# Kernel optimization log

Hardware: AMD Instinct MI355X
Metric: run time of the kernel (lower is better)

Reference implementation:

```python
import jax, jax.numpy as jnp
import numpy as np

VOCAB = 90000
MAX_ID = 95000
EFFECT_DIM = 758
ADD_DIM = 10
EMBED_DIM = 768  # EFFECT_DIM + ADD_DIM
CTX = 1024
MAX_SYN = 8


def setup_inputs() -> dict:
    key = jax.random.key(0)
    k_ids, k_emb, k_rev, k_tab, k_msk = jax.random.split(key, 5)
    ids = jax.random.randint(k_ids, (CTX,), 0, VOCAB, dtype=jnp.int64)
    W_emb = jax.random.normal(k_emb, (MAX_ID, EFFECT_DIM), dtype=jnp.float32)
    W_rev = jax.random.normal(k_rev, (EMBED_DIM, MAX_ID), dtype=jnp.float32)
    padding = 0.1 * jnp.ones((CTX, ADD_DIM), dtype=jnp.float32)
    # synonym ids live in [VOCAB, MAX_ID); only some slots are active (variable-length lists)
    syn_table = jax.random.randint(k_tab, (MAX_ID, MAX_SYN), VOCAB, MAX_ID, dtype=jnp.int32)
    syn_mask = jax.random.randint(k_msk, (MAX_ID, MAX_SYN), 0, 2, dtype=jnp.int32)
    # tokens >= VOCAB (synonym ids themselves) have no synonyms
    syn_mask = syn_mask.at[VOCAB:].set(0)
    return {"ids": ids, "W_emb": W_emb, "W_rev": W_rev, "padding": padding,
            "syn_table": syn_table, "syn_mask": syn_mask}


def reference(ids, W_emb, W_rev, padding, syn_table, syn_mask):
    # VirtualEmbedding: base gather + masked synonym gather/scale/accumulate.
    # i_sum is computed BEFORE the synonym loop in the original, so each
    # synonym contribution is independent -> vectorized masked reduction.
    # (Dropout in eval mode is the identity.)
    base = W_emb[ids]                              # [L, D]
    syn_ids = syn_table[ids]                       # [L, K]
    syn = W_emb[syn_ids]                           # [L, K, D]
    mask = syn_mask[ids].astype(base.dtype)        # [L, K]
    i_sum = jnp.sum(base, axis=-1, keepdims=True)  # [L, 1]
    s_sum = jnp.sum(syn, axis=-1)                  # [L, K]
    d = i_sum / s_sum                              # [L, K]
    emb = base + jnp.einsum('lk,lkd->ld', mask * d, syn)
    # concat fixed context padding, then ReverseEmbedding projection to vocab
    full = jnp.concatenate([emb, padding], axis=1)  # [L, EMBED_DIM]
    return full @ W_rev                             # [L, MAX_ID]
```

## Files before the change

kernel.cpp:

```cpp
#include <hip/hip_runtime.h>
#include <stdint.h>

#define EFFECT_DIM 758
#define ADD_DIM 10
#define EMBED_DIM 768
#define NCOLS 95000
#define NSYN 8
#define NROWS 1024
#define NTILE_N 743

typedef __attribute__((ext_vector_type(8))) __bf16 bf16x8;
typedef __attribute__((ext_vector_type(16))) float f32x16;
typedef __attribute__((ext_vector_type(4))) uint32_t u32x4;

static __device__ __forceinline__ uint32_t pack2(float a, float b) {
  uint32_t r;
  asm("v_cvt_pk_bf16_f32 %0, %1, %2" : "=v"(r) : "v"(a), "v"(b));
  return r;
}

__global__ __launch_bounds__(256) void emb_kernel(
    const int* __restrict__ ids, const float* __restrict__ W_emb,
    const float* __restrict__ padding, const int* __restrict__ syn_table,
    const int* __restrict__ syn_mask, char* __restrict__ ws)
{
  const int l = blockIdx.x;
  const int t = threadIdx.x;
  const int id = ids[l];
  int sid[NSYN];
  int msk[NSYN];
#pragma unroll
  for (int k = 0; k < NSYN; ++k) {
    sid[k] = syn_table[id * NSYN + k];
    msk[k] = syn_mask[id * NSYN + k];
  }

  double p[9] = {0, 0, 0, 0, 0, 0, 0, 0, 0};
  for (int d = t; d < EFFECT_DIM; d += 256) {
    p[0] += (double)W_emb[(size_t)id * EFFECT_DIM + d];
#pragma unroll
    for (int k = 0; k < NSYN; ++k)
      p[k + 1] += (double)W_emb[(size_t)sid[k] * EFFECT_DIM + d];
  }

  __shared__ double s_red[9][4];
  const int w = t >> 6;
#pragma unroll
  for (int k = 0; k < 9; ++k) {
    double v = p[k];
#pragma unroll
    for (int off = 32; off > 0; off >>= 1) v += __shfl_down(v, off, 64);
    if ((t & 63) == 0) s_red[k][w] = v;
  }
  __syncthreads();

  const double isum = s_red[0][0] + s_red[0][1] + s_red[0][2] + s_red[0][3];
  float coef[NSYN];
#pragma unroll
  for (int k = 0; k < NSYN; ++k) {
    double ss = s_red[k + 1][0] + s_red[k + 1][1] + s_red[k + 1][2] + s_red[k + 1][3];
    coef[k] = msk[k] ? (float)(isum / ss) : 0.0f;
  }

  const int mt = l >> 7;
  const int r  = l & 127;
  const int sw = (r & 7) << 4;
  char* wbase = ws + (size_t)mt * (12 * 16384);

  for (int j = t; j < 384; j += 256) {
    const int d0 = 2 * j;
    float v0, v1;
    if (d0 < EFFECT_DIM) {
      const float* bp = W_emb + (size_t)id * EFFECT_DIM + d0;
      v0 = bp[0];
      v1 = bp[1];
#pragma unroll
      for (int k = 0; k < NSYN; ++k) {
        const float* sp = W_emb + (size_t)sid[k] * EFFECT_DIM + d0;
        v0 = fmaf(coef[k], sp[0], v0);
        v1 = fmaf(coef[k], sp[1], v1);
      }
    } else {
      v0 = padding[l * ADD_DIM + (d0 - EFFECT_DIM)];
      v1 = padding[l * ADD_DIM + (d0 + 1 - EFFECT_DIM)];
    }
    const int ks = j >> 5;
    const int jl = j & 31;
    *(uint32_t*)(wbase + ks * 16384 + r * 128 + ((jl * 4) ^ sw)) = pack2(v0, v1);
  }
}

__global__ __launch_bounds__(256) void conv_kernel(
    const float* __restrict__ Wrev, char* __restrict__ Bbuf)
{
  __shared__ char lds[16384];
  const int t  = threadIdx.x;
  const int nt = blockIdx.x;
  const int ks = blockIdx.y;

  const int nl = t & 127;
  const int kc_base = t >> 7;
  const int gn = nt * 128 + nl;
  const bool valid = gn < NCOLS;
  const int sw = (nl & 7) << 4;

#pragma unroll
  for (int task = 0; task < 4; ++task) {
    const int kc = kc_base + task * 2;
    float v[8];
    const float* p = Wrev + (size_t)(ks * 64 + kc * 8) * NCOLS + gn;
#pragma unroll
    for (int j = 0; j < 8; ++j)
      v[j] = valid ? p[(size_t)j * NCOLS] : 0.0f;
    u32x4 u;
#pragma unroll
    for (int j = 0; j < 4; ++j)
      u[j] = pack2(v[2 * j], v[2 * j + 1]);
    *(u32x4*)(lds + nl * 128 + ((kc * 16) ^ sw)) = u;
  }
  __syncthreads();

  char* dst = Bbuf + (size_t)(nt * 12 + ks) * 16384;
#pragma unroll
  for (int i = 0; i < 4; ++i)
    *(u32x4*)(dst + t * 16 + i * 4096) = *(const u32x4*)(lds + t * 16 + i * 4096);
}

__global__ __launch_bounds__(256, 4) void gemm_pre(
    const char* __restrict__ Abuf, const char* __restrict__ Bbuf,
    float* __restrict__ out)
{
  __shared__ char lds[32768];
  const int t  = threadIdx.x;
  const int l  = t & 63;
  const int w  = t >> 6;
  const int wm = w >> 1;
  const int wn = w & 1;
  const int lr = l & 31;
  const int lh = l >> 5;
  const int mt = blockIdx.x;
  const int nt = blockIdx.y;
  const int n0 = nt * 128;

  f32x16 acc[2][2] = {};

  const char* asrc = Abuf + (size_t)mt * (12 * 16384);
  const char* bsrc = Bbuf + (size_t)nt * (12 * 16384);

  for (int ks = 0; ks < 12; ++ks) {
    {
      const char* sa = asrc + ks * 16384 + w * 1024 + l * 16;
      const char* sb = bsrc + ks * 16384 + w * 1024 + l * 16;
      char* da = lds + w * 1024;
      char* db = lds + 16384 + w * 1024;
#pragma unroll
      for (int i = 0; i < 4; ++i) {
        __builtin_amdgcn_global_load_lds(
            (const __attribute__((address_space(1))) uint32_t*)(sa + i * 4096),
            (__attribute__((address_space(3))) uint32_t*)(da + i * 4096),
            16, 0, 0);
        __builtin_amdgcn_global_load_lds(
            (const __attribute__((address_space(1))) uint32_t*)(sb + i * 4096),
            (__attribute__((address_space(3))) uint32_t*)(db + i * 4096),
            16, 0, 0);
      }
    }
    __syncthreads();

    bf16x8 af[2][4], bg[2][4];
#pragma unroll
    for (int mr = 0; mr < 2; ++mr) {
      const int rr = wm * 64 + mr * 32 + lr;
      const int swz = (rr & 7) << 4;
#pragma unroll
      for (int kk = 0; kk < 4; ++kk) {
        const int c2 = kk * 32 + lh * 16;
        af[mr][kk] = *(const bf16x8*)(lds + rr * 128 + (c2 ^ swz));
      }
    }
#pragma unroll
    for (int nr = 0; nr < 2; ++nr) {
      const int rr = wn * 64 + nr * 32 + lr;
      const int swz = (rr & 7) << 4;
#pragma unroll
      for (int kk = 0; kk < 4; ++kk) {
        const int c2 = kk * 32 + lh * 16;
        bg[nr][kk] = *(const bf16x8*)(lds + 16384 + rr * 128 + (c2 ^ swz));
      }
    }
#pragma unroll
    for (int kk = 0; kk < 4; ++kk)
#pragma unroll
      for (int mr = 0; mr < 2; ++mr)
#pragma unroll
        for (int nr = 0; nr < 2; ++nr)
          acc[mr][nr] = __builtin_amdgcn_mfma_f32_32x32x16_bf16(
              af[mr][kk], bg[nr][kk], acc[mr][nr], 0, 0, 0);
    __syncthreads();
  }

#pragma unroll
  for (int mr = 0; mr < 2; ++mr)
#pragma unroll
    for (int nr = 0; nr < 2; ++nr) {
      const int gc = n0 + wn * 64 + nr * 32 + lr;
      if (gc < NCOLS) {
#pragma unroll
        for (int reg = 0; reg < 16; ++reg) {
          const int row = (reg & 3) + 8 * (reg >> 2) + 4 * lh;
          const int gr = mt * 128 + wm * 64 + mr * 32 + row;
          out[(size_t)gr * NCOLS + gc] = acc[mr][nr][reg];
        }
      }
    }
}

__global__ __launch_bounds__(256, 2) void gemm_kernel(
    const float* __restrict__ Wrev, const char* __restrict__ Abuf,
    float* __restrict__ out)
{
  __shared__ char lds[32768];
  const int t  = threadIdx.x;
  const int l  = t & 63;
  const int w  = t >> 6;
  const int wm = w >> 1;
  const int wn = w & 1;
  const int lr = l & 31;
  const int lh = l >> 5;
  const int mt = blockIdx.x;
  const int n0 = blockIdx.y * 128;

  f32x16 acc[2][2] = {};

  const char* asrc = Abuf + (size_t)mt * (12 * 16384);
  const int nl = t & 127;
  const int kc_base = t >> 7;
  const int gn = n0 + nl;
  const int bswz = (nl & 7) << 4;

  for (int ks = 0; ks < 12; ++ks) {
    {
      const char* s = asrc + ks * 16384 + w * 1024 + l * 16;
      char* d = lds + w * 1024;
#pragma unroll
      for (int i = 0; i < 4; ++i) {
        __builtin_amdgcn_global_load_lds(
            (const __attribute__((address_space(1))) uint32_t*)(s + i * 4096),
            (__attribute__((address_space(3))) uint32_t*)(d + i * 4096),
            16, 0, 0);
      }
    }
#pragma unroll
    for (int task = 0; task < 4; ++task) {
      const int kc = kc_base + task * 2;
      float v[8];
      const float* p = Wrev + (size_t)(ks * 64 + kc * 8) * NCOLS + gn;
#pragma unroll
      for (int j = 0; j < 8; ++j)
        v[j] = (gn < NCOLS) ? p[(size_t)j * NCOLS] : 0.0f;
      u32x4 u;
#pragma unroll
      for (int j = 0; j < 4; ++j)
        u[j] = pack2(v[2 * j], v[2 * j + 1]);
      *(u32x4*)(lds + 16384 + nl * 128 + ((kc * 16) ^ bswz)) = u;
    }
    __syncthreads();

    bf16x8 af[2][4], bg[2][4];
#pragma unroll
    for (int mr = 0; mr < 2; ++mr) {
      const int rr = wm * 64 + mr * 32 + lr;
      const int swz = (rr & 7) << 4;
#pragma unroll
      for (int kk = 0; kk < 4; ++kk) {
        const int c2 = kk * 32 + lh * 16;
        af[mr][kk] = *(const bf16x8*)(lds + rr * 128 + (c2 ^ swz));
      }
    }
#pragma unroll
    for (int nr = 0; nr < 2; ++nr) {
      const int rr = wn * 64 + nr * 32 + lr;
      const int swz = (rr & 7) << 4;
#pragma unroll
      for (int kk = 0; kk < 4; ++kk) {
        const int c2 = kk * 32 + lh * 16;
        bg[nr][kk] = *(const bf16x8*)(lds + 16384 + rr * 128 + (c2 ^ swz));
      }
    }
#pragma unroll
    for (int kk = 0; kk < 4; ++kk)
#pragma unroll
      for (int mr = 0; mr < 2; ++mr)
#pragma unroll
        for (int nr = 0; nr < 2; ++nr)
          acc[mr][nr] = __builtin_amdgcn_mfma_f32_32x32x16_bf16(
              af[mr][kk], bg[nr][kk], acc[mr][nr], 0, 0, 0);
    __syncthreads();
  }

#pragma unroll
  for (int mr = 0; mr < 2; ++mr)
#pragma unroll
    for (int nr = 0; nr < 2; ++nr) {
      const int gc = n0 + wn * 64 + nr * 32 + lr;
      if (gc < NCOLS) {
#pragma unroll
        for (int reg = 0; reg < 16; ++reg) {
          const int row = (reg & 3) + 8 * (reg >> 2) + 4 * lh;
          const int gr = mt * 128 + wm * 64 + mr * 32 + row;
          out[(size_t)gr * NCOLS + gc] = acc[mr][nr][reg];
        }
      }
    }
}

extern "C" void kernel_launch(void* const* d_in, const int* in_sizes, int n_in,
                              void* d_out, int out_size, void* d_ws, size_t ws_size,
                              hipStream_t stream) {
  const int*   ids       = (const int*)d_in[0];
  const float* W_emb     = (const float*)d_in[1];
  const float* W_rev     = (const float*)d_in[2];
  const float* padding   = (const float*)d_in[3];
  const int*   syn_table = (const int*)d_in[4];
  const int*   syn_mask  = (const int*)d_in[5];
  float* out = (float*)d_out;
  char*  ws  = (char*)d_ws;

  const size_t A_BYTES = (size_t)8 * 12 * 16384;
  const size_t B_BYTES = (size_t)NTILE_N * 12 * 16384;

  hipLaunchKernelGGL(emb_kernel, dim3(NROWS), dim3(256), 0, stream,
                     ids, W_emb, padding, syn_table, syn_mask, ws);

  if (ws_size >= A_BYTES + B_BYTES) {
    char* Bbuf = ws + A_BYTES;
    hipLaunchKernelGGL(conv_kernel, dim3(NTILE_N, 12), dim3(256), 0, stream,
                       W_rev, Bbuf);
    hipLaunchKernelGGL(gemm_pre, dim3(8, NTILE_N), dim3(256), 0, stream,
                       ws, Bbuf, out);
  } else {
    hipLaunchKernelGGL(gemm_kernel, dim3(8, NTILE_N), dim3(256), 0, stream,
                       W_rev, ws, out);
  }
}
```

Measured before the change: 357.2 us.

## Double-buffer LDS in pre-converted GEMM and remap workgroups per XCD

The pre-converted GEMM now keeps two LDS stages, so the async global-to-LDS load for the next K-step is issued before the current step's MFMAs, with explicit vmcnt waits and raw barriers in place of syncthreads. It also boosts wave priority around the MFMA block and uses a 1D grid whose IDs are remapped so that workgroups on one XCD share neighbouring N tiles and the same A tiles, for better L2 reuse. The larger LDS footprint lowers the occupancy bound from 4 to 2 blocks per CU, which could offset the overlap gain.

```diff
diff --git a/kernel.cpp b/kernel.cpp
--- a/kernel.cpp
+++ b/kernel.cpp
@@ -18,6 +18,11 @@
   asm("v_cvt_pk_bf16_f32 %0, %1, %2" : "=v"(r) : "v"(a), "v"(b));
   return r;
 }
+
+#define GLOAD16(src, dst)                                                   \
+  __builtin_amdgcn_global_load_lds(                                         \
+      (const __attribute__((address_space(1))) uint32_t*)(src),             \
+      (__attribute__((address_space(3))) uint32_t*)(dst), 16, 0, 0)
 
 __global__ __launch_bounds__(256) void emb_kernel(
     const int* __restrict__ ids, const float* __restrict__ W_emb,
@@ -126,11 +131,11 @@
     *(u32x4*)(dst + t * 16 + i * 4096) = *(const u32x4*)(lds + t * 16 + i * 4096);
 }
 
-__global__ __launch_bounds__(256, 4) void gemm_pre(
+__global__ __launch_bounds__(256, 2) void gemm_pre(
     const char* __restrict__ Abuf, const char* __restrict__ Bbuf,
     float* __restrict__ out)
 {
-  __shared__ char lds[32768];
+  __shared__ char lds[65536];
   const int t  = threadIdx.x;
   const int l  = t & 63;
   const int w  = t >> 6;
@@ -138,34 +143,45 @@
   const int wn = w & 1;
   const int lr = l & 31;
   const int lh = l >> 5;
-  const int mt = blockIdx.x;
-  const int nt = blockIdx.y;
+
+  const int wgid = blockIdx.x;
+  const int xcd  = wgid & 7;
+  const int work = xcd * 743 + (wgid >> 3);
+  const int mt = work & 7;
+  const int nt = work >> 3;
   const int n0 = nt * 128;
 
   f32x16 acc[2][2] = {};
 
   const char* asrc = Abuf + (size_t)mt * (12 * 16384);
   const char* bsrc = Bbuf + (size_t)nt * (12 * 16384);
+  const int soff = w * 1024 + l * 16;
+
+#define STAGE(buf, ksi)                                                      \
+  {                                                                          \
+    const char* sa = asrc + (ksi)*16384 + soff;                              \
+    const char* sb = bsrc + (ksi)*16384 + soff;                              \
+    char* da = lds + (buf)*32768 + w * 1024;                                 \
+    char* db = lds + (buf)*32768 + 16384 + w * 1024;                         \
+    _Pragma("unroll") for (int i = 0; i < 4; ++i) {                          \
+      GLOAD16(sa + i * 4096, da + i * 4096);                                 \
+      GLOAD16(sb + i * 4096, db + i * 4096);                                 \
+    }                                                                        \
+  }
+
+  STAGE(0, 0);
 
   for (int ks = 0; ks < 12; ++ks) {
-    {
-      const char* sa = asrc + ks * 16384 + w * 1024 + l * 16;
-      const char* sb = bsrc + ks * 16384 + w * 1024 + l * 16;
-      char* da = lds + w * 1024;
-      char* db = lds + 16384 + w * 1024;
-#pragma unroll
-      for (int i = 0; i < 4; ++i) {
-        __builtin_amdgcn_global_load_lds(
-            (const __attribute__((address_space(1))) uint32_t*)(sa + i * 4096),
-            (__attribute__((address_space(3))) uint32_t*)(da + i * 4096),
-            16, 0, 0);
-        __builtin_amdgcn_global_load_lds(
-            (const __attribute__((address_space(1))) uint32_t*)(sb + i * 4096),
-            (__attribute__((address_space(3))) uint32_t*)(db + i * 4096),
-            16, 0, 0);
-      }
-    }
-    __syncthreads();
+    if (ks < 11) {
+      STAGE((ks + 1) & 1, ks + 1);
+      asm volatile("s_waitcnt vmcnt(8)");
+    } else {
+      asm volatile("s_waitcnt vmcnt(0)");
+    }
+    __builtin_amdgcn_sched_barrier(0);
+    __builtin_amdgcn_s_barrier();
+
+    const char* base = lds + (ks & 1) * 32768;
 
     bf16x8 af[2][4], bg[2][4];
 #pragma unroll
@@ -175,7 +191,7 @@
 #pragma unroll
       for (int kk = 0; kk < 4; ++kk) {
         const int c2 = kk * 32 + lh * 16;
-        af[mr][kk] = *(const bf16x8*)(lds + rr * 128 + (c2 ^ swz));
+        af[mr][kk] = *(const bf16x8*)(base + rr * 128 + (c2 ^ swz));
       }
     }
 #pragma unroll
@@ -185,9 +201,10 @@
 #pragma unroll
       for (int kk = 0; kk < 4; ++kk) {
         const int c2 = kk * 32 + lh * 16;
-        bg[nr][kk] = *(const bf16x8*)(lds + 16384 + rr * 128 + (c2 ^ swz));
-      }
-    }
+        bg[nr][kk] = *(const bf16x8*)(base + 16384 + rr * 128 + (c2 ^ swz));
+      }
+    }
+    __builtin_amdgcn_s_setprio(1);
 #pragma unroll
     for (int kk = 0; kk < 4; ++kk)
 #pragma unroll
@@ -196,8 +213,10 @@
         for (int nr = 0; nr < 2; ++nr)
           acc[mr][nr] = __builtin_amdgcn_mfma_f32_32x32x16_bf16(
               af[mr][kk], bg[nr][kk], acc[mr][nr], 0, 0, 0);
-    __syncthreads();
-  }
+    __builtin_amdgcn_s_setprio(0);
+    __builtin_amdgcn_s_barrier();
+  }
+#undef STAGE
 
 #pragma unroll
   for (int mr = 0; mr < 2; ++mr)
@@ -243,12 +262,8 @@
       const char* s = asrc + ks * 16384 + w * 1024 + l * 16;
       char* d = lds + w * 1024;
 #pragma unroll
-      for (int i = 0; i < 4; ++i) {
-        __builtin_amdgcn_global_load_lds(
-            (const __attribute__((address_space(1))) uint32_t*)(s + i * 4096),
-            (__attribute__((address_space(3))) uint32_t*)(d + i * 4096),
-            16, 0, 0);
-      }
+      for (int i = 0; i < 4; ++i)
+        GLOAD16(s + i * 4096, d + i * 4096);
     }
 #pragma unroll
     for (int task = 0; task < 4; ++task) {
@@ -336,7 +351,7 @@
     char* Bbuf = ws + A_BYTES;
     hipLaunchKernelGGL(conv_kernel, dim3(NTILE_N, 12), dim3(256), 0, stream,
                        W_rev, Bbuf);
-    hipLaunchKernelGGL(gemm_pre, dim3(8, NTILE_N), dim3(256), 0, stream,
+    hipLaunchKernelGGL(gemm_pre, dim3(8 * NTILE_N), dim3(256), 0, stream,
                        ws, Bbuf, out);
   } else {
     hipLaunchKernelGGL(gemm_kernel, dim3(8, NTILE_N), dim3(256), 0, stream,
```

New measurement: 376.6 us. +5.4%, slower.
